# Kernel tuning notes

Hardware: AMD Instinct MI355X
Metric: run time of the kernel (lower is better)

The kernel has to match this reference:

```python
import jax, jax.numpy as jnp
import numpy as np

IMG_W = 224
STRIDE = 16
NUM_HEADS = 12
# 196 grid centers, x-major order: [(x, y) for x in ... for y in ...]
_xs = np.arange(STRIDE // 2, IMG_W, STRIDE)
GRIDS = jnp.asarray(np.array([(x, y) for x in _xs for y in _xs], dtype=np.float32))  # [196, 2]


def setup_inputs() -> dict:
    key = jax.random.key(0)
    ks = jax.random.split(key, 8)
    B, N, C = 256, 198, 768
    s = 0.02
    return {
        "x": jax.random.normal(ks[0], (B, N, C), dtype=jnp.float32),
        "w_qkv": jax.random.normal(ks[1], (C, 3 * C), dtype=jnp.float32) * s,  # qkv_bias=False
        "w_proj": jax.random.normal(ks[2], (C, C), dtype=jnp.float32) * s,
        "b_proj": jax.random.normal(ks[3], (C,), dtype=jnp.float32) * s,
        "w_D": jax.random.normal(ks[4], (C, 3), dtype=jnp.float32) * s,
        "b_D": jax.random.normal(ks[5], (3,), dtype=jnp.float32) * s,
        "w_cen": jax.random.normal(ks[6], (C, 6), dtype=jnp.float32) * s,
        "b_cen": jax.random.normal(ks[7], (6,), dtype=jnp.float32) * s,
    }


def reference(x, w_qkv, w_proj, b_proj, w_D, b_D, w_cen, b_cen):
    B, N, C = x.shape
    H = NUM_HEADS
    dh = C // H
    scale = dh ** (-0.5)

    qkv = (x @ w_qkv).reshape(B, N, 3, H, dh).transpose(2, 0, 3, 1, 4)  # [3,B,H,N,dh]
    q, k, v = qkv[0], qkv[1], qkv[2]

    attn = jnp.einsum('bhnd,bhmd->bhnm', q, k) * scale
    attn = jax.nn.softmax(attn, axis=-1)  # [B,H,N,N]

    # CLS-token query, heads concatenated: q.permute(2,0,1,3).reshape(N,B,C)[0]
    q0 = q[:, :, 0, :].reshape(B, C)
    D = IMG_W * jax.nn.sigmoid(q0 @ w_D + b_D)                      # [B,3]
    cen = jax.nn.sigmoid((q0 @ w_cen + b_cen).reshape(B, 3, 2))     # [B,3,2]

    # mixture-of-gaussian blobs over 196 patch grid positions
    sigma = (D / 2.0)[..., None]                                    # [B,3,1]
    coord = cen * (IMG_W - 1)                                       # [B,3,2]
    dist = ((coord[:, :, None, :] - GRIDS[None, None]) ** 2).sum(-1)  # [B,3,196]
    mgb = jnp.exp(-dist / (2.0 * sigma ** 2)) / 2.0 / 3.14 / sigma ** 2
    mgb = mgb / mgb.sum(-1, keepdims=True)
    mgb = mgb.sum(axis=1) / 3.0                                     # [B,196]
    mgb = jnp.concatenate([jnp.ones((B, 2), mgb.dtype), mgb], axis=1)  # [B,N]

    # head-score reweighting of the CLS attention row
    hs = attn[:, :, 0, :].transpose(1, 0, 2)   # [H,B,N] == permute(1,2,0,3) squeezed
    hs = hs * mgb[None]                        # broadcast over heads
    hs = hs / hs.sum(-1, keepdims=True)
    # replicate torch masked_scatter flat-order semantics:
    # source flattened in (h,b,n) order is written into target positions in (b,h,n) order
    new_row = hs.reshape(-1).reshape(B, H, N)
    attn = attn.at[:, :, 0, :].set(new_row)

    out = jnp.einsum('bhnm,bhmd->bhnd', attn, v)      # [B,H,N,dh]
    out = out.transpose(0, 2, 1, 3).reshape(B, N, C)
    out = out @ w_proj + b_proj
    return cen, attn[:, :, 0, :], out
```

## Files before the change

kernel.cpp:

```cpp
#include <hip/hip_runtime.h>
#include <cstdint>
#include <cstddef>

typedef __attribute__((ext_vector_type(4))) float  f32x4;
typedef __attribute__((ext_vector_type(8))) __bf16 bf16x8;
typedef __attribute__((ext_vector_type(4))) __bf16 bf16x4;

#define MFMA16(A, B, C) __builtin_amdgcn_mfma_f32_16x16x32_bf16((A), (B), (C), 0, 0, 0)

#define GLOAD_LDS16(gp, lp)                                        \
    __builtin_amdgcn_global_load_lds(                              \
        (const __attribute__((address_space(1))) void*)(gp),       \
        (__attribute__((address_space(3))) void*)(lp), 16, 0, 0)

#define NB 256
#define NN 198
#define NC 768
#define NH 12

__global__ __launch_bounds__(256) void cast_to_bf16(const float* __restrict__ in,
                                                    __bf16* __restrict__ out, int n8) {
    int i = blockIdx.x * 256 + threadIdx.x;
    if (i < n8) {
        const float4 f0 = reinterpret_cast<const float4*>(in)[i * 2];
        const float4 f1 = reinterpret_cast<const float4*>(in)[i * 2 + 1];
        bf16x8 h;
        h[0] = (__bf16)f0.x; h[1] = (__bf16)f0.y; h[2] = (__bf16)f0.z; h[3] = (__bf16)f0.w;
        h[4] = (__bf16)f1.x; h[5] = (__bf16)f1.y; h[6] = (__bf16)f1.z; h[7] = (__bf16)f1.w;
        reinterpret_cast<bf16x8*>(out)[i] = h;
    }
}

__global__ void transpose_to_bf16(const float* __restrict__ in, __bf16* __restrict__ out,
                                  int R, int Cc) {
    int idx = blockIdx.x * 256 + threadIdx.x;
    if (idx < R * Cc) {
        int r = idx / Cc, c = idx % Cc;
        out[(size_t)c * R + r] = (__bf16)in[idx];
    }
}

__global__ __launch_bounds__(256) void gemm_qkv_v4(
    const __bf16* __restrict__ xb, const __bf16* __restrict__ wT,
    __bf16* __restrict__ qb, __bf16* __restrict__ kb, __bf16* __restrict__ vb,
    float* __restrict__ q0) {
    __shared__ __bf16 As[4][128 * 32];
    __shared__ __bf16 Bs[4][128 * 32];
    const int bid = blockIdx.x;
    const int wg  = (bid & 7) * 891 + (bid >> 3);
    const int brow = (wg / 18) * 128;
    const int bcol = (wg % 18) * 128;
    const int tid = threadIdx.x, lane = tid & 63, wid = tid >> 6;
    const int wm = wid >> 1, wn = wid & 1;
    const int lr = lane & 15, lg = lane >> 4;

    const int srow = wid * 32 + (lane >> 2);
    const int scol = (((lane & 3) ^ ((lane >> 3) & 3)) * 8);
    const __bf16* aSrc = xb + (size_t)(brow + srow) * 768 + scol;
    const __bf16* bSrc = wT + (size_t)(bcol + srow) * 768 + scol;
    const int rkey = (lr >> 1) & 3;

    f32x4 acc[4][4] = {};

#define STAGE_Q(buf, kk)                                                      \
    {                                                                         \
        __bf16* aD = &As[buf][wid * 1024];                                    \
        __bf16* bD = &Bs[buf][wid * 1024];                                    \
        GLOAD_LDS16(aSrc + (kk), aD);                                         \
        GLOAD_LDS16(bSrc + (kk), bD);                                         \
        GLOAD_LDS16(aSrc + (size_t)16 * 768 + (kk), aD + 512);                \
        GLOAD_LDS16(bSrc + (size_t)16 * 768 + (kk), bD + 512);                \
    }

#define COMPUTE_Q(buf)                                                        \
    {                                                                         \
        const __bf16* Ab = As[buf];                                           \
        const __bf16* Bb = Bs[buf];                                           \
        bf16x8 af[4], bfv[4];                                                 \
        _Pragma("unroll")                                                     \
        for (int mt = 0; mt < 4; ++mt)                                        \
            af[mt] = *reinterpret_cast<const bf16x8*>(                        \
                Ab + (wm * 64 + mt * 16 + lr) * 32 + ((lg ^ rkey) * 8));      \
        _Pragma("unroll")                                                     \
        for (int nt = 0; nt < 4; ++nt)                                        \
            bfv[nt] = *reinterpret_cast<const bf16x8*>(                       \
                Bb + (wn * 64 + nt * 16 + lr) * 32 + ((lg ^ rkey) * 8));      \
        __builtin_amdgcn_s_setprio(1);                                        \
        _Pragma("unroll")                                                     \
        for (int mt = 0; mt < 4; ++mt)                                        \
            _Pragma("unroll")                                                 \
            for (int nt = 0; nt < 4; ++nt)                                    \
                acc[mt][nt] = MFMA16(af[mt], bfv[nt], acc[mt][nt]);           \
        __builtin_amdgcn_s_setprio(0);                                        \
    }

    STAGE_Q(0, 0);
    STAGE_Q(1, 32);
    STAGE_Q(2, 64);
    for (int t = 0; t < 22; ++t) {
        asm volatile("s_waitcnt vmcnt(8)" ::: "memory");
        __builtin_amdgcn_s_barrier();
        __builtin_amdgcn_sched_barrier(0);
        if (t < 21) STAGE_Q((t + 3) & 3, (t + 3) * 32);
        COMPUTE_Q(t & 3);
    }
    asm volatile("s_waitcnt vmcnt(4)" ::: "memory");
    __builtin_amdgcn_s_barrier();
    __builtin_amdgcn_sched_barrier(0);
    COMPUTE_Q(2);
    asm volatile("s_waitcnt vmcnt(0)" ::: "memory");
    __builtin_amdgcn_s_barrier();
    __builtin_amdgcn_sched_barrier(0);
    COMPUTE_Q(3);
#undef STAGE_Q
#undef COMPUTE_Q

#pragma unroll
    for (int mt = 0; mt < 4; ++mt) {
        int grow0 = brow + wm * 64 + mt * 16 + lg * 4;
#pragma unroll
        for (int nt = 0; nt < 4; ++nt) {
            int gcol = bcol + wn * 64 + nt * 16 + lr;
            int sidx = gcol / 768;
            int rem  = gcol % 768;
            __bf16* dstbuf = (sidx == 0) ? qb : (sidx == 1) ? kb : vb;
            int hh = rem >> 6, dd = rem & 63;
#pragma unroll
            for (int r = 0; r < 4; ++r) {
                int grow = grow0 + r;
                int bb = grow / 198, nn2 = grow % 198;
                float val = acc[mt][nt][r];
                dstbuf[(((size_t)bb * 12 + hh) * 198 + nn2) * 64 + dd] = (__bf16)val;
                if (sidx == 0 && nn2 == 0) q0[bb * 768 + rem] = val;
            }
        }
    }
}

__global__ __launch_bounds__(256) void mgb_kernel(
    const float* __restrict__ q0, const float* __restrict__ wD,
    const float* __restrict__ bD, const float* __restrict__ wcen,
    const float* __restrict__ bcen, float* __restrict__ cen_out,
    float* __restrict__ mgb) {
    const int b = blockIdx.x, t = threadIdx.x;
    __shared__ float qs[768];
    __shared__ float red[256];
    __shared__ float vals[9];
    qs[t]       = q0[b * 768 + t];
    qs[t + 256] = q0[b * 768 + t + 256];
    qs[t + 512] = q0[b * 768 + t + 512];
    __syncthreads();
    for (int j = 0; j < 9; ++j) {
        float p;
        if (j < 3)
            p = qs[t] * wD[t * 3 + j] + qs[t + 256] * wD[(t + 256) * 3 + j] +
                qs[t + 512] * wD[(t + 512) * 3 + j];
        else {
            int c = j - 3;
            p = qs[t] * wcen[t * 6 + c] + qs[t + 256] * wcen[(t + 256) * 6 + c] +
                qs[t + 512] * wcen[(t + 512) * 6 + c];
        }
        red[t] = p;
        __syncthreads();
        for (int off = 128; off > 0; off >>= 1) {
            if (t < off) red[t] += red[t + off];
            __syncthreads();
        }
        if (t == 0) {
            float bias = (j < 3) ? bD[j] : bcen[j - 3];
            vals[j] = 1.f / (1.f + __expf(-(red[0] + bias)));
        }
        __syncthreads();
    }
    if (t < 6) cen_out[b * 6 + t] = vals[3 + t];

    float e3[3] = {0.f, 0.f, 0.f};
    if (t < 196) {
        float gx = 8.f + 16.f * (float)(t / 14);
        float gy = 8.f + 16.f * (float)(t % 14);
#pragma unroll
        for (int j = 0; j < 3; ++j) {
            float sig = 112.f * vals[j];
            float cx = vals[3 + 2 * j] * 223.f;
            float cy = vals[3 + 2 * j + 1] * 223.f;
            float dx = cx - gx, dy = cy - gy;
            e3[j] = __expf(-(dx * dx + dy * dy) / (2.f * sig * sig));
        }
    }
    float js[3];
    for (int j = 0; j < 3; ++j) {
        red[t] = e3[j];
        __syncthreads();
        for (int off = 128; off > 0; off >>= 1) {
            if (t < off) red[t] += red[t + off];
            __syncthreads();
        }
        js[j] = red[0];
        __syncthreads();
    }
    if (t < 196) {
        float m = (e3[0] / js[0] + e3[1] / js[1] + e3[2] / js[2]) * (1.f / 3.f);
        mgb[(size_t)b * 198 + 2 + t] = m;
    }
    if (t < 2) mgb[(size_t)b * 198 + t] = 1.f;
}

__global__ __launch_bounds__(256) void attn_kernel(
    const __bf16* __restrict__ qb, const __bf16* __restrict__ kb,
    const __bf16* __restrict__ vb, float* __restrict__ p0,
    __bf16* __restrict__ outp) {
    __shared__ __bf16 Vt[64][216];
    __shared__ __bf16 Plds[4][16][216];
    const int bh = blockIdx.x;
    const int b = bh / 12, h = bh % 12;
    const __bf16* Qp = qb + (size_t)bh * NN * 64;
    const __bf16* Kp = kb + (size_t)bh * NN * 64;
    const __bf16* Vp = vb + (size_t)bh * NN * 64;
    const int tid = threadIdx.x, lane = tid & 63, wid = tid >> 6;
    const int lr = lane & 15, lg = lane >> 4;

    for (int i = tid; i < 208 * 8; i += 256) {
        int key = i >> 3, d0 = (i & 7) << 3;
        int krow = key < 198 ? key : 197;
        bf16x8 hv = *reinterpret_cast<const bf16x8*>(Vp + krow * 64 + d0);
#pragma unroll
        for (int j = 0; j < 8; ++j) Vt[d0 + j][key] = hv[j];
    }
    __syncthreads();

    for (int ch = wid; ch < 13; ch += 4) {
        int n0 = ch * 16;
        int qrow = n0 + lr; if (qrow > 197) qrow = 197;
        bf16x8 qf0 = *reinterpret_cast<const bf16x8*>(Qp + qrow * 64 + lg * 8);
        bf16x8 qf1 = *reinterpret_cast<const bf16x8*>(Qp + qrow * 64 + 32 + lg * 8);
        f32x4 sa[13];
#pragma unroll
        for (int t2 = 0; t2 < 13; ++t2) {
            int krow = t2 * 16 + lr; if (krow > 197) krow = 197;
            bf16x8 kf0 = *reinterpret_cast<const bf16x8*>(Kp + krow * 64 + lg * 8);
            bf16x8 kf1 = *reinterpret_cast<const bf16x8*>(Kp + krow * 64 + 32 + lg * 8);
            f32x4 a = (f32x4){0.f, 0.f, 0.f, 0.f};
            a = MFMA16(kf0, qf0, a);
            a = MFMA16(kf1, qf1, a);
            sa[t2] = a;
        }
        float rmax = -1e30f;
#pragma unroll
        for (int t2 = 0; t2 < 13; ++t2)
#pragma unroll
            for (int r = 0; r < 4; ++r) {
                int key = t2 * 16 + lg * 4 + r;
                float vv = (key < 198) ? sa[t2][r] * 0.125f : -1e30f;
                sa[t2][r] = vv;
                rmax = fmaxf(rmax, vv);
            }
        rmax = fmaxf(rmax, __shfl_xor(rmax, 16));
        rmax = fmaxf(rmax, __shfl_xor(rmax, 32));
        float rsum = 0.f;
#pragma unroll
        for (int t2 = 0; t2 < 13; ++t2)
#pragma unroll
            for (int r = 0; r < 4; ++r) {
                float e = __expf(sa[t2][r] - rmax);
                sa[t2][r] = e;
                rsum += e;
            }
        rsum += __shfl_xor(rsum, 16);
        rsum += __shfl_xor(rsum, 32);
        float inv = 1.f / rsum;

        if (ch == 0 && lr == 0) {
#pragma unroll
            for (int t2 = 0; t2 < 13; ++t2)
#pragma unroll
                for (int r = 0; r < 4; ++r) {
                    int key = t2 * 16 + lg * 4 + r;
                    if (key < 198) p0[(size_t)bh * 198 + key] = sa[t2][r] * inv;
                }
        }
#pragma unroll
        for (int t2 = 0; t2 < 13; ++t2) {
            bf16x4 pk;
#pragma unroll
            for (int r = 0; r < 4; ++r) pk[r] = (__bf16)(sa[t2][r] * inv);
            *reinterpret_cast<bf16x4*>(&Plds[wid][lr][t2 * 16 + lg * 4]) = pk;
        }
        asm volatile("s_waitcnt lgkmcnt(0)" ::: "memory");

        f32x4 o[4];
#pragma unroll
        for (int mt = 0; mt < 4; ++mt) o[mt] = (f32x4){0.f, 0.f, 0.f, 0.f};
#pragma unroll
        for (int ks = 0; ks < 7; ++ks) {
            int kbase = ks * 32 + lg * 8;
            bf16x8 pf;
            if (kbase < 208)
                pf = *reinterpret_cast<const bf16x8*>(&Plds[wid][lr][kbase]);
            else {
#pragma unroll
                for (int j = 0; j < 8; ++j) pf[j] = (__bf16)0.f;
            }
#pragma unroll
            for (int mt = 0; mt < 4; ++mt) {
                bf16x8 vf;
                if (kbase < 208)
                    vf = *reinterpret_cast<const bf16x8*>(&Vt[mt * 16 + lr][kbase]);
                else {
#pragma unroll
                    for (int j = 0; j < 8; ++j) vf[j] = (__bf16)0.f;
                }
                o[mt] = MFMA16(vf, pf, o[mt]);
            }
        }
        int qg = n0 + lr;
        if (qg < 198) {
            __bf16* dst = outp + ((size_t)b * 198 + qg) * 768 + h * 64;
#pragma unroll
            for (int mt = 0; mt < 4; ++mt) {
                bf16x4 pk;
#pragma unroll
                for (int r = 0; r < 4; ++r) pk[r] = (__bf16)o[mt][r];
                *reinterpret_cast<bf16x4*>(dst + mt * 16 + lg * 4) = pk;
            }
        }
    }
}

__global__ __launch_bounds__(64) void reweight_kernel(
    const float* __restrict__ p0, const float* __restrict__ mgb,
    const __bf16* __restrict__ vb, float* __restrict__ attn_out,
    __bf16* __restrict__ outp) {
    const int t = blockIdx.x;
    const int b = t / 12, h = t % 12;
    const int h2 = t >> 8, b2 = t & 255;
    const int lane = threadIdx.x;
    __shared__ float nr[198];
    const float* pr = p0 + (size_t)(b2 * 12 + h2) * 198;
    const float* mr = mgb + (size_t)b2 * 198;
    float w[4];
    float ssum = 0.f;
#pragma unroll
    for (int i = 0; i < 4; ++i) {
        int n = lane + 64 * i;
        float xv = (n < 198) ? pr[n] * mr[n] : 0.f;
        w[i] = xv;
        ssum += xv;
    }
#pragma unroll
    for (int m = 1; m < 64; m <<= 1) ssum += __shfl_xor(ssum, m);
    float inv = 1.f / ssum;
#pragma unroll
    for (int i = 0; i < 4; ++i) {
        int n = lane + 64 * i;
        if (n < 198) {
            float xv = w[i] * inv;
            nr[n] = xv;
            attn_out[(size_t)t * 198 + n] = xv;
        }
    }
    __syncthreads();
    const __bf16* vp = vb + (size_t)t * 198 * 64;
    float acc = 0.f;
    for (int n = 0; n < 198; ++n) acc += nr[n] * (float)vp[n * 64 + lane];
    outp[((size_t)b * 198) * 768 + h * 64 + lane] = (__bf16)acc;
}

__global__ __launch_bounds__(256) void gemm_proj_v4(
    const __bf16* __restrict__ A, const __bf16* __restrict__ wT,
    const float* __restrict__ bias, float* __restrict__ out) {
    __shared__ __bf16 As[4][128 * 32];
    __shared__ __bf16 Bs[4][128 * 32];
    const int bid = blockIdx.x;
    const int wg  = (bid & 7) * 297 + (bid >> 3);
    const int brow = (wg / 6) * 128;
    const int bcol = (wg % 6) * 128;
    const int tid = threadIdx.x, lane = tid & 63, wid = tid >> 6;
    const int wm = wid >> 1, wn = wid & 1;
    const int lr = lane & 15, lg = lane >> 4;

    const int srow = wid * 32 + (lane >> 2);
    const int scol = (((lane & 3) ^ ((lane >> 3) & 3)) * 8);
    const __bf16* aSrc = A  + (size_t)(brow + srow) * 768 + scol;
    const __bf16* bSrc = wT + (size_t)(bcol + srow) * 768 + scol;
    const int rkey = (lr >> 1) & 3;

    f32x4 acc[4][4] = {};

#define STAGE_P(buf, kk)                                                      \
    {                                                                         \
        __bf16* aD = &As[buf][wid * 1024];                                    \
        __bf16* bD = &Bs[buf][wid * 1024];                                    \
        GLOAD_LDS16(aSrc + (kk), aD);                                         \
        GLOAD_LDS16(bSrc + (kk), bD);                                         \
        GLOAD_LDS16(aSrc + (size_t)16 * 768 + (kk), aD + 512);                \
        GLOAD_LDS16(bSrc + (size_t)16 * 768 + (kk), bD + 512);                \
    }

#define COMPUTE_P(buf)                                                        \
    {                                                                         \
        const __bf16* Ab = As[buf];                                           \
        const __bf16* Bb = Bs[buf];                                           \
        bf16x8 af[4], bfv[4];                                                 \
        _Pragma("unroll")                                                     \
        for (int mt = 0; mt < 4; ++mt)                                        \
            af[mt] = *reinterpret_cast<const bf16x8*>(                        \
                Ab + (wm * 64 + mt * 16 + lr) * 32 + ((lg ^ rkey) * 8));      \
        _Pragma("unroll")                                                     \
        for (int nt = 0; nt < 4; ++nt)                                        \
            bfv[nt] = *reinterpret_cast<const bf16x8*>(                       \
                Bb + (wn * 64 + nt * 16 + lr) * 32 + ((lg ^ rkey) * 8));      \
        __builtin_amdgcn_s_setprio(1);                                        \
        _Pragma("unroll")                                                     \
        for (int mt = 0; mt < 4; ++mt)                                        \
            _Pragma("unroll")                                                 \
            for (int nt = 0; nt < 4; ++nt)                                    \
                acc[mt][nt] = MFMA16(af[mt], bfv[nt], acc[mt][nt]);           \
        __builtin_amdgcn_s_setprio(0);                                        \
    }

    STAGE_P(0, 0);
    STAGE_P(1, 32);
    STAGE_P(2, 64);
    for (int t = 0; t < 22; ++t) {
        asm volatile("s_waitcnt vmcnt(8)" ::: "memory");
        __builtin_amdgcn_s_barrier();
        __builtin_amdgcn_sched_barrier(0);
        if (t < 21) STAGE_P((t + 3) & 3, (t + 3) * 32);
        COMPUTE_P(t & 3);
    }
    asm volatile("s_waitcnt vmcnt(4)" ::: "memory");
    __builtin_amdgcn_s_barrier();
    __builtin_amdgcn_sched_barrier(0);
    COMPUTE_P(2);
    asm volatile("s_waitcnt vmcnt(0)" ::: "memory");
    __builtin_amdgcn_s_barrier();
    __builtin_amdgcn_sched_barrier(0);
    COMPUTE_P(3);
#undef STAGE_P
#undef COMPUTE_P

#pragma unroll
    for (int mt = 0; mt < 4; ++mt) {
#pragma unroll
        for (int nt = 0; nt < 4; ++nt) {
            int gcol = bcol + wn * 64 + nt * 16 + lr;
            float bv = bias[gcol];
#pragma unroll
            for (int r = 0; r < 4; ++r) {
                int grow = brow + wm * 64 + mt * 16 + lg * 4 + r;
                out[(size_t)grow * 768 + gcol] = acc[mt][nt][r] + bv;
            }
        }
    }
}

extern "C" void kernel_launch(void* const* d_in, const int* in_sizes, int n_in,
                              void* d_out, int out_size, void* d_ws, size_t ws_size,
                              hipStream_t stream) {
    const float* x      = (const float*)d_in[0];
    const float* w_qkv  = (const float*)d_in[1];
    const float* w_proj = (const float*)d_in[2];
    const float* b_proj = (const float*)d_in[3];
    const float* w_D    = (const float*)d_in[4];
    const float* b_D    = (const float*)d_in[5];
    const float* w_cen  = (const float*)d_in[6];
    const float* b_cen  = (const float*)d_in[7];

    float* out      = (float*)d_out;
    float* cen_out  = out;
    float* attn_out = out + 1536;
    float* proj_out = out + 1536 + 608256;

    char* ws = (char*)d_ws;
    size_t off = 0;
    auto carve = [&](size_t bytes) {
        void* p = ws + off;
        off += (bytes + 255) & ~(size_t)255;
        return p;
    };
    __bf16* wqkvT  = (__bf16*)carve((size_t)2304 * 768 * 2);
    __bf16* wprojT = (__bf16*)carve((size_t)768 * 768 * 2);
    __bf16* qb     = (__bf16*)carve((size_t)3072 * 198 * 64 * 2);
    __bf16* kb     = (__bf16*)carve((size_t)3072 * 198 * 64 * 2);
    __bf16* vb     = (__bf16*)carve((size_t)3072 * 198 * 64 * 2);
    __bf16* outp   = (__bf16*)carve((size_t)50688 * 768 * 2);
    float*  q0     = (float*)carve((size_t)256 * 768 * 4);
    float*  mgb    = (float*)carve((size_t)256 * 198 * 4);
    float*  p0     = (float*)carve((size_t)3072 * 198 * 4);

    __bf16* xb = outp;

    cast_to_bf16<<<(50688 * 768 / 8 + 255) / 256, 256, 0, stream>>>(x, xb, 50688 * 768 / 8);
    transpose_to_bf16<<<(768 * 2304 + 255) / 256, 256, 0, stream>>>(w_qkv, wqkvT, 768, 2304);
    transpose_to_bf16<<<(768 * 768 + 255) / 256, 256, 0, stream>>>(w_proj, wprojT, 768, 768);
    gemm_qkv_v4<<<7128, 256, 0, stream>>>(xb, wqkvT, qb, kb, vb, q0);
    mgb_kernel<<<256, 256, 0, stream>>>(q0, w_D, b_D, w_cen, b_cen, cen_out, mgb);
    attn_kernel<<<3072, 256, 0, stream>>>(qb, kb, vb, p0, outp);
    reweight_kernel<<<3072, 64, 0, stream>>>(p0, mgb, vb, attn_out, outp);
    gemm_proj_v4<<<2376, 256, 0, stream>>>(outp, wprojT, b_proj, proj_out);
}
```

Measured before the change: 616.0 us.

## Switch QKV and proj GEMMs to double-buffered LDS with higher occupancy

Both bf16 MFMA GEMMs move from a 4-stage LDS ring with three tiles prefetched to a 2-stage double buffer. This halves shared memory per block (64KB to 32KB), and launch_bounds(256,3) requests three resident blocks per CU. The aim is to hide latency through more concurrent workgroups rather than deep prefetch. The staging pattern changes so each thread loads rows tid/4 and tid/4+64, and B fragments are read before A. An extra barrier per K-step guards buffer reuse, which costs some synchronization and leaves less prefetch depth per block.

```diff
diff --git a/kernel.cpp b/kernel.cpp
--- a/kernel.cpp
+++ b/kernel.cpp
@@ -40,12 +40,12 @@
     }
 }
 
-__global__ __launch_bounds__(256) void gemm_qkv_v4(
+__global__ __launch_bounds__(256, 3) void gemm_qkv_v6(
     const __bf16* __restrict__ xb, const __bf16* __restrict__ wT,
     __bf16* __restrict__ qb, __bf16* __restrict__ kb, __bf16* __restrict__ vb,
     float* __restrict__ q0) {
-    __shared__ __bf16 As[4][128 * 32];
-    __shared__ __bf16 Bs[4][128 * 32];
+    __shared__ __bf16 As[2][128 * 32];
+    __shared__ __bf16 Bs[2][128 * 32];
     const int bid = blockIdx.x;
     const int wg  = (bid & 7) * 891 + (bid >> 3);
     const int brow = (wg / 18) * 128;
@@ -54,22 +54,22 @@
     const int wm = wid >> 1, wn = wid & 1;
     const int lr = lane & 15, lg = lane >> 4;
 
-    const int srow = wid * 32 + (lane >> 2);
-    const int scol = (((lane & 3) ^ ((lane >> 3) & 3)) * 8);
-    const __bf16* aSrc = xb + (size_t)(brow + srow) * 768 + scol;
-    const __bf16* bSrc = wT + (size_t)(bcol + srow) * 768 + scol;
+    const int srow = tid >> 2;
+    const int sslot = (tid & 3) ^ ((tid >> 3) & 3);
+    const __bf16* aSrc = xb + (size_t)(brow + srow) * 768 + sslot * 8;
+    const __bf16* bSrc = wT + (size_t)(bcol + srow) * 768 + sslot * 8;
     const int rkey = (lr >> 1) & 3;
 
     f32x4 acc[4][4] = {};
 
-#define STAGE_Q(buf, kk)                                                      \
+#define STAGE_Q(buf, kk0)                                                     \
     {                                                                         \
-        __bf16* aD = &As[buf][wid * 1024];                                    \
-        __bf16* bD = &Bs[buf][wid * 1024];                                    \
-        GLOAD_LDS16(aSrc + (kk), aD);                                         \
-        GLOAD_LDS16(bSrc + (kk), bD);                                         \
-        GLOAD_LDS16(aSrc + (size_t)16 * 768 + (kk), aD + 512);                \
-        GLOAD_LDS16(bSrc + (size_t)16 * 768 + (kk), bD + 512);                \
+        __bf16* aD = &As[buf][wid * 512];                                     \
+        __bf16* bD = &Bs[buf][wid * 512];                                     \
+        GLOAD_LDS16(aSrc + (kk0), aD);                                        \
+        GLOAD_LDS16(bSrc + (kk0), bD);                                        \
+        GLOAD_LDS16(aSrc + (size_t)64 * 768 + (kk0), aD + 2048);              \
+        GLOAD_LDS16(bSrc + (size_t)64 * 768 + (kk0), bD + 2048);              \
     }
 
 #define COMPUTE_Q(buf)                                                        \
@@ -78,13 +78,13 @@
         const __bf16* Bb = Bs[buf];                                           \
         bf16x8 af[4], bfv[4];                                                 \
         _Pragma("unroll")                                                     \
+        for (int nt = 0; nt < 4; ++nt)                                        \
+            bfv[nt] = *reinterpret_cast<const bf16x8*>(                       \
+                Bb + (wn * 64 + nt * 16 + lr) * 32 + ((lg ^ rkey) * 8));      \
+        _Pragma("unroll")                                                     \
         for (int mt = 0; mt < 4; ++mt)                                        \
             af[mt] = *reinterpret_cast<const bf16x8*>(                        \
                 Ab + (wm * 64 + mt * 16 + lr) * 32 + ((lg ^ rkey) * 8));      \
-        _Pragma("unroll")                                                     \
-        for (int nt = 0; nt < 4; ++nt)                                        \
-            bfv[nt] = *reinterpret_cast<const bf16x8*>(                       \
-                Bb + (wn * 64 + nt * 16 + lr) * 32 + ((lg ^ rkey) * 8));      \
         __builtin_amdgcn_s_setprio(1);                                        \
         _Pragma("unroll")                                                     \
         for (int mt = 0; mt < 4; ++mt)                                        \
@@ -96,22 +96,17 @@
 
     STAGE_Q(0, 0);
     STAGE_Q(1, 32);
-    STAGE_Q(2, 64);
-    for (int t = 0; t < 22; ++t) {
-        asm volatile("s_waitcnt vmcnt(8)" ::: "memory");
+    for (int tau = 0; tau < 24; ++tau) {
+        if (tau == 23) asm volatile("s_waitcnt vmcnt(0)" ::: "memory");
+        else           asm volatile("s_waitcnt vmcnt(4)" ::: "memory");
         __builtin_amdgcn_s_barrier();
         __builtin_amdgcn_sched_barrier(0);
-        if (t < 21) STAGE_Q((t + 3) & 3, (t + 3) * 32);
-        COMPUTE_Q(t & 3);
-    }
-    asm volatile("s_waitcnt vmcnt(4)" ::: "memory");
-    __builtin_amdgcn_s_barrier();
-    __builtin_amdgcn_sched_barrier(0);
-    COMPUTE_Q(2);
-    asm volatile("s_waitcnt vmcnt(0)" ::: "memory");
-    __builtin_amdgcn_s_barrier();
-    __builtin_amdgcn_sched_barrier(0);
-    COMPUTE_Q(3);
+        COMPUTE_Q(tau & 1);
+        __builtin_amdgcn_sched_barrier(0);
+        __builtin_amdgcn_s_barrier();
+        __builtin_amdgcn_sched_barrier(0);
+        if (tau < 22) STAGE_Q(tau & 1, (tau + 2) * 32);
+    }
 #undef STAGE_Q
 #undef COMPUTE_Q
 
@@ -365,11 +360,11 @@
     outp[((size_t)b * 198) * 768 + h * 64 + lane] = (__bf16)acc;
 }
 
-__global__ __launch_bounds__(256) void gemm_proj_v4(
+__global__ __launch_bounds__(256, 3) void gemm_proj_v6(
     const __bf16* __restrict__ A, const __bf16* __restrict__ wT,
     const float* __restrict__ bias, float* __restrict__ out) {
-    __shared__ __bf16 As[4][128 * 32];
-    __shared__ __bf16 Bs[4][128 * 32];
+    __shared__ __bf16 As[2][128 * 32];
+    __shared__ __bf16 Bs[2][128 * 32];
     const int bid = blockIdx.x;
     const int wg  = (bid & 7) * 297 + (bid >> 3);
     const int brow = (wg / 6) * 128;
@@ -378,22 +373,22 @@
     const int wm = wid >> 1, wn = wid & 1;
     const int lr = lane & 15, lg = lane >> 4;
 
-    const int srow = wid * 32 + (lane >> 2);
-    const int scol = (((lane & 3) ^ ((lane >> 3) & 3)) * 8);
-    const __bf16* aSrc = A  + (size_t)(brow + srow) * 768 + scol;
-    const __bf16* bSrc = wT + (size_t)(bcol + srow) * 768 + scol;
+    const int srow = tid >> 2;
+    const int sslot = (tid & 3) ^ ((tid >> 3) & 3);
+    const __bf16* aSrc = A  + (size_t)(brow + srow) * 768 + sslot * 8;
+    const __bf16* bSrc = wT + (size_t)(bcol + srow) * 768 + sslot * 8;
     const int rkey = (lr >> 1) & 3;
 
     f32x4 acc[4][4] = {};
 
-#define STAGE_P(buf, kk)                                                      \
+#define STAGE_P(buf, kk0)                                                     \
     {                                                                         \
-        __bf16* aD = &As[buf][wid * 1024];                                    \
-        __bf16* bD = &Bs[buf][wid * 1024];                                    \
-        GLOAD_LDS16(aSrc + (kk), aD);                                         \
-        GLOAD_LDS16(bSrc + (kk), bD);                                         \
-        GLOAD_LDS16(aSrc + (size_t)16 * 768 + (kk), aD + 512);                \
-        GLOAD_LDS16(bSrc + (size_t)16 * 768 + (kk), bD + 512);                \
+        __bf16* aD = &As[buf][wid * 512];                                     \
+        __bf16* bD = &Bs[buf][wid * 512];                                     \
+        GLOAD_LDS16(aSrc + (kk0), aD);                                        \
+        GLOAD_LDS16(bSrc + (kk0), bD);                                        \
+        GLOAD_LDS16(aSrc + (size_t)64 * 768 + (kk0), aD + 2048);              \
+        GLOAD_LDS16(bSrc + (size_t)64 * 768 + (kk0), bD + 2048);              \
     }
 
 #define COMPUTE_P(buf)                                                        \
@@ -402,13 +397,13 @@
         const __bf16* Bb = Bs[buf];                                           \
         bf16x8 af[4], bfv[4];                                                 \
         _Pragma("unroll")                                                     \
+        for (int nt = 0; nt < 4; ++nt)                                        \
+            bfv[nt] = *reinterpret_cast<const bf16x8*>(                       \
+                Bb + (wn * 64 + nt * 16 + lr) * 32 + ((lg ^ rkey) * 8));      \
+        _Pragma("unroll")                                                     \
         for (int mt = 0; mt < 4; ++mt)                                        \
             af[mt] = *reinterpret_cast<const bf16x8*>(                        \
                 Ab + (wm * 64 + mt * 16 + lr) * 32 + ((lg ^ rkey) * 8));      \
-        _Pragma("unroll")                                                     \
-        for (int nt = 0; nt < 4; ++nt)                                        \
-            bfv[nt] = *reinterpret_cast<const bf16x8*>(                       \
-                Bb + (wn * 64 + nt * 16 + lr) * 32 + ((lg ^ rkey) * 8));      \
         __builtin_amdgcn_s_setprio(1);                                        \
         _Pragma("unroll")                                                     \
         for (int mt = 0; mt < 4; ++mt)                                        \
@@ -420,22 +415,17 @@
 
     STAGE_P(0, 0);
     STAGE_P(1, 32);
-    STAGE_P(2, 64);
-    for (int t = 0; t < 22; ++t) {
-        asm volatile("s_waitcnt vmcnt(8)" ::: "memory");
+    for (int tau = 0; tau < 24; ++tau) {
+        if (tau == 23) asm volatile("s_waitcnt vmcnt(0)" ::: "memory");
+        else           asm volatile("s_waitcnt vmcnt(4)" ::: "memory");
         __builtin_amdgcn_s_barrier();
         __builtin_amdgcn_sched_barrier(0);
-        if (t < 21) STAGE_P((t + 3) & 3, (t + 3) * 32);
-        COMPUTE_P(t & 3);
-    }
-    asm volatile("s_waitcnt vmcnt(4)" ::: "memory");
-    __builtin_amdgcn_s_barrier();
-    __builtin_amdgcn_sched_barrier(0);
-    COMPUTE_P(2);
-    asm volatile("s_waitcnt vmcnt(0)" ::: "memory");
-    __builtin_amdgcn_s_barrier();
-    __builtin_amdgcn_sched_barrier(0);
-    COMPUTE_P(3);
+        COMPUTE_P(tau & 1);
+        __builtin_amdgcn_sched_barrier(0);
+        __builtin_amdgcn_s_barrier();
+        __builtin_amdgcn_sched_barrier(0);
+        if (tau < 22) STAGE_P(tau & 1, (tau + 2) * 32);
+    }
 #undef STAGE_P
 #undef COMPUTE_P
 
@@ -493,9 +483,9 @@
     cast_to_bf16<<<(50688 * 768 / 8 + 255) / 256, 256, 0, stream>>>(x, xb, 50688 * 768 / 8);
     transpose_to_bf16<<<(768 * 2304 + 255) / 256, 256, 0, stream>>>(w_qkv, wqkvT, 768, 2304);
     transpose_to_bf16<<<(768 * 768 + 255) / 256, 256, 0, stream>>>(w_proj, wprojT, 768, 768);
-    gemm_qkv_v4<<<7128, 256, 0, stream>>>(xb, wqkvT, qb, kb, vb, q0);
+    gemm_qkv_v6<<<7128, 256, 0, stream>>>(xb, wqkvT, qb, kb, vb, q0);
     mgb_kernel<<<256, 256, 0, stream>>>(q0, w_D, b_D, w_cen, b_cen, cen_out, mgb);
     attn_kernel<<<3072, 256, 0, stream>>>(qb, kb, vb, p0, outp);
     reweight_kernel<<<3072, 64, 0, stream>>>(p0, mgb, vb, attn_out, outp);
-    gemm_proj_v4<<<2376, 256, 0, stream>>>(outp, wprojT, b_proj, proj_out);
-}
+    gemm_proj_v6<<<2376, 256, 0, stream>>>(outp, wprojT, b_proj, proj_out);
+}
```

Result: faster. 580.9 us (-5.7%).
